# Kernel tuning notes

Hardware: AMD Instinct MI355X
Metric: run time of the kernel (lower is better)

The kernel has to match this reference:

```python
import jax, jax.numpy as jnp
import numpy as np

T, B, E, H = 2048, 2, 1024, 16
HD = E // H
NEG = -1e9  # large negative for causal additive mask


def setup_inputs() -> dict:
    key = jax.random.key(0)
    ks = jax.random.split(key, 6)
    s = 0.02
    query = jax.random.normal(ks[0], (T, B, E), jnp.float32)
    # causal additive mask, as commonly passed to this module's attn_mask arg
    attn_mask = jnp.triu(jnp.full((T, T), NEG, jnp.float32), k=1)
    key_padding_mask = jnp.zeros((B, T), jnp.bool_)
    Wq = jax.random.normal(ks[1], (E, E), jnp.float32) * s
    Wk = jax.random.normal(ks[2], (E, E), jnp.float32) * s
    Wv = jax.random.normal(ks[3], (E, E), jnp.float32) * s
    Wo = jax.random.normal(ks[4], (E, E), jnp.float32) * s
    bq = jnp.zeros((E,), jnp.float32)
    bk = jnp.zeros((E,), jnp.float32)
    bv = jnp.zeros((E,), jnp.float32)
    bo = jnp.zeros((E,), jnp.float32)
    return {"query": query, "attn_mask": attn_mask, "key_padding_mask": key_padding_mask,
            "Wq": Wq, "bq": bq, "Wk": Wk, "bk": bk, "Wv": Wv, "bv": bv, "Wo": Wo, "bo": bo}


def _shape(x):
    # [T, B, E] -> [B*H, T, HD]; E splits as (H, HD), flat index = b*H + h
    return x.reshape(T, B * H, HD).transpose(1, 0, 2)


def reference(query, attn_mask, key_padding_mask, Wq, bq, Wk, bk, Wv, bv, Wo, bo):
    scaling = HD ** -0.5
    q = (query @ Wq.T + bq) * scaling  # scale q as in torch code
    k = query @ Wk.T + bk              # self-attention path (static_kv=False)
    v = query @ Wv.T + bv
    q, k, v = _shape(q), _shape(k), _shape(v)            # [B*H, T, HD]
    w = jnp.einsum('bth,bsh->bts', q, k)                  # [B*H, T, S]
    w = w.reshape(B, H, T, T) + attn_mask                 # additive mask broadcast
    w = jnp.where(key_padding_mask[:, None, None, :], -jnp.inf, w)
    p = jax.nn.softmax(w, axis=-1).reshape(B * H, T, T)   # dropout p=0 (eval)
    o = jnp.einsum('bts,bsh->bth', p, v)                  # [B*H, T, HD]
    o = o.transpose(1, 0, 2).reshape(T, B, E)
    return o @ Wo.T + bo
```

## Files before the change

kernel.cpp:

```cpp
#include <hip/hip_runtime.h>

#define Tt 2048
#define Bb 2
#define Ee 1024
#define Hh 16
#define HD 64
#define BH 32

typedef __attribute__((ext_vector_type(8))) short short8;
typedef __attribute__((ext_vector_type(4))) short short4v;
typedef __attribute__((ext_vector_type(8))) __bf16 bf16x8;
typedef __attribute__((ext_vector_type(4))) float floatx4;

#define OFF_X  0
#define OFF_WQ 4194304
#define OFF_WK 5242880
#define OFF_WV 6291456
#define OFF_WO 7340032
#define OFF_Q  8388608
#define OFF_K  12582912
#define OFF_V  16777216
#define OFF_O  20971520

__device__ __forceinline__ short f2bf(float f) {
  union { float f; unsigned u; } a; a.f = f;
  unsigned r = a.u + 0x7fffu + ((a.u >> 16) & 1u);
  return (short)(r >> 16);
}

__device__ __forceinline__ floatx4 mfma16(short8 a, short8 b, floatx4 c) {
  return __builtin_amdgcn_mfma_f32_16x16x32_bf16(
      __builtin_bit_cast(bf16x8, a), __builtin_bit_cast(bf16x8, b), c, 0, 0, 0);
}

__device__ __forceinline__ void gl_lds16(const short* g, short* l) {
  __builtin_amdgcn_global_load_lds(
      (const __attribute__((address_space(1))) void*)g,
      (__attribute__((address_space(3))) void*)l, 16, 0, 0);
}

__device__ __forceinline__ uint2 exppack(floatx4 s, float& l) {
  float p0 = __builtin_amdgcn_exp2f(s[0]);
  float p1 = __builtin_amdgcn_exp2f(s[1]);
  float p2 = __builtin_amdgcn_exp2f(s[2]);
  float p3 = __builtin_amdgcn_exp2f(s[3]);
  l += (p0 + p1) + (p2 + p3);
  unsigned u0 = __builtin_bit_cast(unsigned, p0) + 0x8000u;
  unsigned u1 = __builtin_bit_cast(unsigned, p1) + 0x8000u;
  unsigned u2 = __builtin_bit_cast(unsigned, p2) + 0x8000u;
  unsigned u3 = __builtin_bit_cast(unsigned, p3) + 0x8000u;
  uint2 pk;
  pk.x = __builtin_amdgcn_perm(u1, u0, 0x07060302u);
  pk.y = __builtin_amdgcn_perm(u3, u2, 0x07060302u);
  return pk;
}

__global__ __launch_bounds__(256)
void convert_kernel(const float* __restrict__ x, const float* __restrict__ wq,
                    const float* __restrict__ wk, const float* __restrict__ wv,
                    const float* __restrict__ wo, short* __restrict__ dst)
{
  const int i4 = blockIdx.x * 256 + threadIdx.x;
  const int f = i4 * 4;
  const float* src;
  int local;
  if (f < 4194304) { src = x; local = f; }
  else {
    int gg = f - 4194304;
    int wsel = gg >> 20;
    local = gg & 1048575;
    src = (wsel == 0) ? wq : (wsel == 1) ? wk : (wsel == 2) ? wv : wo;
  }
  floatx4 v = *reinterpret_cast<const floatx4*>(src + local);
  short4 o;
  o.x = f2bf(v[0]); o.y = f2bf(v[1]); o.z = f2bf(v[2]); o.w = f2bf(v[3]);
  *reinterpret_cast<short4*>(dst + f) = o;
}

__global__ __launch_bounds__(256, 2)
void qkv_kernel(short* __restrict__ ws, const float* __restrict__ bq,
                const float* __restrict__ bk, const float* __restrict__ bv)
{
  __shared__ short smem[2][8192];
  const int t = threadIdx.x;
  const int lane = t & 63;
  const int w = t >> 6;
  const int g = lane >> 4, c = lane & 15;
  const int rb = blockIdx.x * 128;
  const int cb = blockIdx.y * 128;
  const int rw = (w >> 1) * 64, cw2 = (w & 1) * 64;

  const short* gA[2]; const short* gB[2]; int oC[2];
#pragma unroll
  for (int i = 0; i < 2; i++) {
    const int cid = t + 256 * i;
    const int row = cid >> 2;
    const int lch = (cid & 3) ^ ((row + (row >> 2)) & 3);
    gA[i] = ws + OFF_X + (rb + row) * 1024 + lch * 8;
    gB[i] = ws + OFF_WQ + (cb + row) * 1024 + lch * 8;
    oC[i] = cid * 8;
  }
  const int xr = (g ^ ((c + (c >> 2)) & 3)) * 8;

  floatx4 acc[4][4];
#pragma unroll
  for (int i = 0; i < 4; i++)
#pragma unroll
    for (int j = 0; j < 4; j++) acc[i][j] = (floatx4){0.f, 0.f, 0.f, 0.f};

#pragma unroll
  for (int i = 0; i < 2; i++) {
    gl_lds16(gA[i], &smem[0][oC[i]]);
    gl_lds16(gB[i], &smem[0][4096 + oC[i]]);
  }
  __syncthreads();

  for (int kt = 0; kt < 32; kt++) {
    const int cur = kt & 1;
    if (kt < 31) {
      const int kn = (kt + 1) * 32;
#pragma unroll
      for (int i = 0; i < 2; i++) {
        gl_lds16(gA[i] + kn, &smem[cur ^ 1][oC[i]]);
        gl_lds16(gB[i] + kn, &smem[cur ^ 1][4096 + oC[i]]);
      }
    }
    short8 af[4], bf[4];
#pragma unroll
    for (int mi = 0; mi < 4; mi++)
      af[mi] = *reinterpret_cast<const short8*>(&smem[cur][(rw + mi * 16 + c) * 32 + xr]);
#pragma unroll
    for (int ni = 0; ni < 4; ni++)
      bf[ni] = *reinterpret_cast<const short8*>(&smem[cur][4096 + (cw2 + ni * 16 + c) * 32 + xr]);
#pragma unroll
    for (int mi = 0; mi < 4; mi++)
#pragma unroll
      for (int ni = 0; ni < 4; ni++)
        acc[mi][ni] = mfma16(af[mi], bf[ni], acc[mi][ni]);
    __syncthreads();
  }

  const int m = cb >> 10;
  const int lcb = cb & 1023;
  if (m < 2) {
    short* vt = &smem[0][0];
    const float sc = (m == 0) ? 0.18033688f : 1.0f;
    const int baseo = (m == 0) ? OFF_Q : OFF_K;
    for (int hb = 0; hb < 2; hb++) {
      __syncthreads();
      if ((w >> 1) == hb) {
#pragma unroll
        for (int ni = 0; ni < 4; ni++) {
          const int lc = cw2 + ni * 16 + c;
          const float bcol = (m == 0 ? bq : bk)[lcb + lc];
#pragma unroll
          for (int mi = 0; mi < 4; mi++)
#pragma unroll
            for (int r = 0; r < 4; r++)
              vt[(mi * 16 + g * 4 + r) * 136 + lc] = f2bf((acc[mi][ni][r] + bcol) * sc);
        }
      }
      __syncthreads();
#pragma unroll
      for (int i = 0; i < 4; i++) {
        const int u = t + 256 * i;
        const int ttl = u & 31, bsel = (u >> 5) & 1, lc8 = u >> 6;
        const int rl = ttl * 2 + bsel;
        const int row = rb + hb * 64 + rl;
        const int tt = row >> 1, bb = row & 1;
        const int hh = (lcb + lc8 * 8) >> 6;
        short8 vv = *reinterpret_cast<const short8*>(vt + rl * 136 + lc8 * 8);
        *reinterpret_cast<short8*>(ws + baseo + (bb * Hh + hh) * 131072
            + (tt >> 4) * 1024 + (lc8 & 7) * 128 + (tt & 15) * 8) = vv;
      }
    }
  } else {
    short* vt = &smem[0][0];
    const int hb = lcb >> 6;
    for (int b = 0; b < 2; b++) {
      __syncthreads();
#pragma unroll
      for (int ni = 0; ni < 4; ni++) {
        const int lcol = cw2 + ni * 16 + c;
        const float bcol = bv[lcb + lcol];
#pragma unroll
        for (int mi = 0; mi < 4; mi++)
#pragma unroll
          for (int rr = 0; rr < 2; rr++) {
            const int r = rr * 2 + b;
            const int rloc = rw + mi * 16 + g * 4 + r;
            vt[lcol * 72 + (rloc >> 1)] = f2bf(acc[mi][ni][r] + bcol);
          }
      }
      __syncthreads();
#pragma unroll
      for (int i = 0; i < 4; i++) {
        const int u = t + 256 * i;
        const int lcol = u >> 3, seg = u & 7;
        short8 vv = *reinterpret_cast<const short8*>(vt + lcol * 72 + seg * 8);
        const int h = hb + (lcol >> 6), d = lcol & 63;
        *reinterpret_cast<short8*>(ws + OFF_V + ((b * Hh + h)) * 131072
                                   + ((rb >> 5) + (seg >> 1)) * 1024
                                   + d * 16 + (seg & 1) * 8) = vv;
      }
    }
  }
}

__global__ __launch_bounds__(256, 2)
void gemm_o(const short* __restrict__ ws, const float* __restrict__ bo,
            float* __restrict__ dout)
{
  __shared__ short smem[2][8192];
  const int t = threadIdx.x;
  const int lane = t & 63;
  const int w = t >> 6;
  const int g = lane >> 4, c = lane & 15;
  const int rb = blockIdx.x * 128;
  const int cb = blockIdx.y * 128;
  const int rw = (w >> 1) * 64, cw2 = (w & 1) * 64;

  const short* gA[2]; const short* gB[2]; int oC[2];
#pragma unroll
  for (int i = 0; i < 2; i++) {
    const int cid = t + 256 * i;
    const int row = cid >> 2;
    const int lch = (cid & 3) ^ ((row + (row >> 2)) & 3);
    gA[i] = ws + OFF_O + (rb + row) * 1024 + lch * 8;
    gB[i] = ws + OFF_WO + (cb + row) * 1024 + lch * 8;
    oC[i] = cid * 8;
  }
  const int xr = (g ^ ((c + (c >> 2)) & 3)) * 8;

  floatx4 acc[4][4];
#pragma unroll
  for (int i = 0; i < 4; i++)
#pragma unroll
    for (int j = 0; j < 4; j++) acc[i][j] = (floatx4){0.f, 0.f, 0.f, 0.f};

#pragma unroll
  for (int i = 0; i < 2; i++) {
    gl_lds16(gA[i], &smem[0][oC[i]]);
    gl_lds16(gB[i], &smem[0][4096 + oC[i]]);
  }
  __syncthreads();

  for (int kt = 0; kt < 32; kt++) {
    const int cur = kt & 1;
    if (kt < 31) {
      const int kn = (kt + 1) * 32;
#pragma unroll
      for (int i = 0; i < 2; i++) {
        gl_lds16(gA[i] + kn, &smem[cur ^ 1][oC[i]]);
        gl_lds16(gB[i] + kn, &smem[cur ^ 1][4096 + oC[i]]);
      }
    }
    short8 af[4], bf[4];
#pragma unroll
    for (int mi = 0; mi < 4; mi++)
      af[mi] = *reinterpret_cast<const short8*>(&smem[cur][(rw + mi * 16 + c) * 32 + xr]);
#pragma unroll
    for (int ni = 0; ni < 4; ni++)
      bf[ni] = *reinterpret_cast<const short8*>(&smem[cur][4096 + (cw2 + ni * 16 + c) * 32 + xr]);
#pragma unroll
    for (int mi = 0; mi < 4; mi++)
#pragma unroll
      for (int ni = 0; ni < 4; ni++)
        acc[mi][ni] = mfma16(af[mi], bf[ni], acc[mi][ni]);
    __syncthreads();
  }

#pragma unroll
  for (int ni = 0; ni < 4; ni++) {
    const int col = cb + cw2 + ni * 16 + c;
    const float bcol = bo[col];
#pragma unroll
    for (int mi = 0; mi < 4; mi++)
#pragma unroll
      for (int r = 0; r < 4; r++) {
        const int row = rb + rw + mi * 16 + g * 4 + r;
        dout[row * 1024 + col] = acc[mi][ni][r] + bcol;
      }
  }
}

__global__ __launch_bounds__(256, 3)
void attn_kernel(short* __restrict__ ws, const unsigned char* __restrict__ kpm)
{
  __shared__ __align__(16) short smem[24576];

  const int t = threadIdx.x;
  const int lane = t & 63;
  const int w = t >> 6;
  const int g = lane >> 4, c = lane & 15;
  const int bh = blockIdx.x;
  const int b = bh >> 4;
  const int h = bh & 15;
  const int qt = 31 - (int)blockIdx.y;
  const int qrow0 = qt * 64;

  const short* Qp = ws + OFF_Q + bh * 131072;
  const short* Kp = ws + OFF_K + bh * 131072;
  const short* Vp = ws + OFF_V + bh * 131072;

  short8 qf[4][2];
  const short* Qc = Qp + (qrow0 >> 4) * 1024 + lane * 8;
#pragma unroll
  for (int qs = 0; qs < 4; qs++) {
    qf[qs][0] = *reinterpret_cast<const short8*>(Qc + qs * 1024);
    qf[qs][1] = *reinterpret_cast<const short8*>(Qc + qs * 1024 + 512);
  }

  const uint4* kpv = reinterpret_cast<const uint4*>(kpm + b * Tt);
  uint4 k0v = kpv[lane * 2], k1v = kpv[lane * 2 + 1];
  const bool nz = (k0v.x | k0v.y | k0v.z | k0v.w | k1v.x | k1v.y | k1v.z | k1v.w) != 0;
  const unsigned long long kpany = __ballot(nz);

  float lt[4] = {0.f, 0.f, 0.f, 0.f};
  floatx4 acc[4][4];
#pragma unroll
  for (int i = 0; i < 4; i++)
#pragma unroll
    for (int j = 0; j < 4; j++) acc[i][j] = (floatx4){0.f, 0.f, 0.f, 0.f};

  const short* Ksrc = Kp + w * 1024 + lane * 8;
  const short* Vsrc = Vp + w * 1024 + lane * 8;
  const int woff = w * 1024;

  const int NT = qt + 1;
  const int NP = (NT + 1) >> 1;

  gl_lds16(Ksrc,       &smem[woff]);
  gl_lds16(Ksrc + 512, &smem[woff + 512]);
  gl_lds16(Vsrc,       &smem[4096 + woff]);
  gl_lds16(Vsrc + 512, &smem[4096 + woff + 512]);
  if (NT > 1) {
    gl_lds16(Ksrc + 4096,       &smem[8192 + woff]);
    gl_lds16(Ksrc + 4096 + 512, &smem[8192 + woff + 512]);
    gl_lds16(Vsrc + 4096,       &smem[8192 + 4096 + woff]);
    gl_lds16(Vsrc + 4096 + 512, &smem[8192 + 4096 + 512 + woff]);
  }

  int co = 0;
  for (int pp = 0; pp < NP; pp++) {
    const int ta = 2 * pp, tb = ta + 1;
    int cbuf = co + 8192;  if (cbuf >= 24576) cbuf -= 24576;
    int cn   = co + 16384; if (cn   >= 24576) cn   -= 24576;

    if (ta + 2 < NT) {
      const short* ks = Ksrc + (ta + 2) * 4096;
      const short* vs = Vsrc + (ta + 2) * 4096;
      gl_lds16(ks,       &smem[cn + woff]);
      gl_lds16(ks + 512, &smem[cn + woff + 512]);
      gl_lds16(vs,       &smem[cn + 4096 + woff]);
      gl_lds16(vs + 512, &smem[cn + 4096 + woff + 512]);
      asm volatile("s_waitcnt vmcnt(8)" ::: "memory");
    } else if (tb < NT) {
      asm volatile("s_waitcnt vmcnt(4)" ::: "memory");
    } else {
      asm volatile("s_waitcnt vmcnt(0)" ::: "memory");
    }
    __builtin_amdgcn_sched_barrier(0);

    const short* kfa = &smem[co + woff + g * 128 + c * 8];
    short8 ka0 = *reinterpret_cast<const short8*>(kfa);
    short8 ka1 = *reinterpret_cast<const short8*>(kfa + 512);
    __builtin_amdgcn_s_setprio(1);
    floatx4 sa[4];
#pragma unroll
    for (int qs = 0; qs < 4; qs++) {
      floatx4 z = (floatx4){0.f, 0.f, 0.f, 0.f};
      z = mfma16(ka0, qf[qs][0], z);
      z = mfma16(ka1, qf[qs][1], z);
      sa[qs] = z;
    }
    __builtin_amdgcn_s_setprio(0);
    if ((kpany >> (2 * ta)) & 3ULL) {
#pragma unroll
      for (int r = 0; r < 4; r++)
        if (kpm[b * Tt + ta * 64 + w * 16 + g * 4 + r] != 0) {
#pragma unroll
          for (int qs = 0; qs < 4; qs++) sa[qs][r] = -1e30f;
        }
    }
    if (ta == qt) {
      const int kl = w * 16 + g * 4;
#pragma unroll
      for (int qs = 0; qs < 4; qs++)
#pragma unroll
        for (int r = 0; r < 4; r++)
          if (kl + r > qs * 16 + c) sa[qs][r] = -1e30f;
    }
    uint2 ua[4];
#pragma unroll
    for (int qs = 0; qs < 4; qs++) ua[qs] = exppack(sa[qs], lt[qs]);
    const short* vfa = &smem[co + 4096 + woff + c * 16 + g * 4];
    short4v vA[4];
#pragma unroll
    for (int dt = 0; dt < 4; dt++)
      vA[dt] = *reinterpret_cast<const short4v*>(vfa + dt * 256);

    uint2 ub[4];
    ub[0] = ub[1] = ub[2] = ub[3] = (uint2){0u, 0u};
    short4v vB[4];
#pragma unroll
    for (int dt = 0; dt < 4; dt++) vB[dt] = vA[dt];
    if (tb < NT) {
      if (tb + 2 < NT) {
        const short* ks = Ksrc + (tb + 2) * 4096;
        const short* vs = Vsrc + (tb + 2) * 4096;
        gl_lds16(ks,       &smem[co + woff]);
        gl_lds16(ks + 512, &smem[co + woff + 512]);
        gl_lds16(vs,       &smem[co + 4096 + woff]);
        gl_lds16(vs + 512, &smem[co + 4096 + woff + 512]);
        asm volatile("s_waitcnt vmcnt(8)" ::: "memory");
      } else if (tb + 1 < NT) {
        asm volatile("s_waitcnt vmcnt(4)" ::: "memory");
      } else {
        asm volatile("s_waitcnt vmcnt(0)" ::: "memory");
      }
      __builtin_amdgcn_sched_barrier(0);

      const short* kfb = &smem[cbuf + woff + g * 128 + c * 8];
      short8 kb0 = *reinterpret_cast<const short8*>(kfb);
      short8 kb1 = *reinterpret_cast<const short8*>(kfb + 512);
      __builtin_amdgcn_s_setprio(1);
      floatx4 sb[4];
#pragma unroll
      for (int qs = 0; qs < 4; qs++) {
        floatx4 z = (floatx4){0.f, 0.f, 0.f, 0.f};
        z = mfma16(kb0, qf[qs][0], z);
        z = mfma16(kb1, qf[qs][1], z);
        sb[qs] = z;
      }
      __builtin_amdgcn_s_setprio(0);
      if ((kpany >> (2 * tb)) & 3ULL) {
#pragma unroll
        for (int r = 0; r < 4; r++)
          if (kpm[b * Tt + tb * 64 + w * 16 + g * 4 + r] != 0) {
#pragma unroll
            for (int qs = 0; qs < 4; qs++) sb[qs][r] = -1e30f;
          }
      }
      if (tb == qt) {
        const int kl = w * 16 + g * 4;
#pragma unroll
        for (int qs = 0; qs < 4; qs++)
#pragma unroll
          for (int r = 0; r < 4; r++)
            if (kl + r > qs * 16 + c) sb[qs][r] = -1e30f;
      }
#pragma unroll
      for (int qs = 0; qs < 4; qs++) ub[qs] = exppack(sb[qs], lt[qs]);
      const short* vfb = &smem[cbuf + 4096 + woff + c * 16 + g * 4];
#pragma unroll
      for (int dt = 0; dt < 4; dt++)
        vB[dt] = *reinterpret_cast<const short4v*>(vfb + dt * 256);
    }

    short8 pa8[4];
#pragma unroll
    for (int qs = 0; qs < 4; qs++) {
      uint4 uu; uu.x = ua[qs].x; uu.y = ua[qs].y; uu.z = ub[qs].x; uu.w = ub[qs].y;
      pa8[qs] = __builtin_bit_cast(short8, uu);
    }
    __builtin_amdgcn_s_setprio(1);
#pragma unroll
    for (int dt = 0; dt < 4; dt++) {
      short8 vv;
      vv[0] = vA[dt][0]; vv[1] = vA[dt][1]; vv[2] = vA[dt][2]; vv[3] = vA[dt][3];
      vv[4] = vB[dt][0]; vv[5] = vB[dt][1]; vv[6] = vB[dt][2]; vv[7] = vB[dt][3];
#pragma unroll
      for (int qs = 0; qs < 4; qs++)
        acc[qs][dt] = mfma16(pa8[qs], vv, acc[qs][dt]);
    }
    __builtin_amdgcn_s_setprio(0);

    co = cn;
  }

#pragma unroll
  for (int qs = 0; qs < 4; qs++) {
    lt[qs] += __shfl_xor(lt[qs], 16);
    lt[qs] += __shfl_xor(lt[qs], 32);
  }

  __syncthreads();
  float* bufA = reinterpret_cast<float*>(smem);
  float* bufB = bufA + 4352;
  float* Ls   = bufA + 8704;
  if (g == 0) {
#pragma unroll
    for (int qs = 0; qs < 4; qs++) Ls[w * 64 + qs * 16 + c] = lt[qs];
  }
  float* mybuf = (w < 2) ? bufA : bufB;
  if ((w & 1) == 0) {
#pragma unroll
    for (int qs = 0; qs < 4; qs++)
#pragma unroll
      for (int dt = 0; dt < 4; dt++)
#pragma unroll
        for (int r = 0; r < 4; r++)
          mybuf[(qs * 16 + g * 4 + r) * 68 + dt * 16 + c] = acc[qs][dt][r];
  }
  __syncthreads();
  if (w & 1) {
#pragma unroll
    for (int qs = 0; qs < 4; qs++)
#pragma unroll
      for (int dt = 0; dt < 4; dt++)
#pragma unroll
        for (int r = 0; r < 4; r++)
          mybuf[(qs * 16 + g * 4 + r) * 68 + dt * 16 + c] += acc[qs][dt][r];
  }
  __syncthreads();

  const int row = w * 16 + (lane >> 2);
  const int dseg = (lane & 3) * 16;
  const float inv = 1.f / (Ls[row] + Ls[64 + row] + Ls[128 + row] + Ls[192 + row]);
  short* op = ws + OFF_O + ((qrow0 + row) * Bb + b) * Ee + h * 64 + dseg;
#pragma unroll
  for (int i = 0; i < 2; i++) {
    floatx4 a0 = *reinterpret_cast<const floatx4*>(&bufA[row * 68 + dseg + i * 8]);
    floatx4 a1 = *reinterpret_cast<const floatx4*>(&bufA[row * 68 + dseg + i * 8 + 4]);
    floatx4 b0 = *reinterpret_cast<const floatx4*>(&bufB[row * 68 + dseg + i * 8]);
    floatx4 b1 = *reinterpret_cast<const floatx4*>(&bufB[row * 68 + dseg + i * 8 + 4]);
    short8 s;
#pragma unroll
    for (int j = 0; j < 4; j++) s[j] = f2bf((a0[j] + b0[j]) * inv);
#pragma unroll
    for (int j = 0; j < 4; j++) s[4 + j] = f2bf((a1[j] + b1[j]) * inv);
    *reinterpret_cast<short8*>(op + i * 8) = s;
  }
}

extern "C" void kernel_launch(void* const* d_in, const int* in_sizes, int n_in,
                              void* d_out, int out_size, void* d_ws, size_t ws_size,
                              hipStream_t stream)
{
  const float* query = (const float*)d_in[0];
  const unsigned char* kpm = (const unsigned char*)d_in[2];
  const float* Wq = (const float*)d_in[3];
  const float* bq = (const float*)d_in[4];
  const float* Wk = (const float*)d_in[5];
  const float* bk = (const float*)d_in[6];
  const float* Wv = (const float*)d_in[7];
  const float* bv = (const float*)d_in[8];
  const float* Wo = (const float*)d_in[9];
  const float* bo = (const float*)d_in[10];
  short* ws = (short*)d_ws;
  float* out = (float*)d_out;

  convert_kernel<<<dim3(8192), dim3(256), 0, stream>>>(query, Wq, Wk, Wv, Wo, ws);
  qkv_kernel<<<dim3(32, 24), dim3(256), 0, stream>>>(ws, bq, bk, bv);
  attn_kernel<<<dim3(32, 32), dim3(256), 0, stream>>>(ws, kpm);
  gemm_o<<<dim3(32, 8), dim3(256), 0, stream>>>(ws, bo, out);
}
```

Baseline: 181.8 us.

## Give each wave private LDS tiles in QKV GEMM to drop block barriers

The QKV projection GEMM now has each wave load its own 64-row A and B slices into a private LDS region, double-buffered, instead of the block sharing 128x32 tiles. This removes the per-iteration __syncthreads and replaces it with s_waitcnt vmcnt on the wave's own async loads. The cost is duplicated global loads (each A/B row is fetched by two waves), a 64KB LDS footprint that may reduce occupancy below the launch bound of 2 blocks, and the loss of the XOR swizzle, which may add LDS bank conflicts.

```diff
diff --git a/kernel.cpp b/kernel.cpp
--- a/kernel.cpp
+++ b/kernel.cpp
@@ -81,7 +81,7 @@
 void qkv_kernel(short* __restrict__ ws, const float* __restrict__ bq,
                 const float* __restrict__ bk, const float* __restrict__ bv)
 {
-  __shared__ short smem[2][8192];
+  __shared__ __align__(16) short smem[32768];
   const int t = threadIdx.x;
   const int lane = t & 63;
   const int w = t >> 6;
@@ -90,17 +90,9 @@
   const int cb = blockIdx.y * 128;
   const int rw = (w >> 1) * 64, cw2 = (w & 1) * 64;
 
-  const short* gA[2]; const short* gB[2]; int oC[2];
-#pragma unroll
-  for (int i = 0; i < 2; i++) {
-    const int cid = t + 256 * i;
-    const int row = cid >> 2;
-    const int lch = (cid & 3) ^ ((row + (row >> 2)) & 3);
-    gA[i] = ws + OFF_X + (rb + row) * 1024 + lch * 8;
-    gB[i] = ws + OFF_WQ + (cb + row) * 1024 + lch * 8;
-    oC[i] = cid * 8;
-  }
-  const int xr = (g ^ ((c + (c >> 2)) & 3)) * 8;
+  const short* srcA = ws + OFF_X  + (rb + rw  + (lane >> 2)) * 1024 + (lane & 3) * 8;
+  const short* srcB = ws + OFF_WQ + (cb + cw2 + (lane >> 2)) * 1024 + (lane & 3) * 8;
+  const int wbase = w * 4096;
 
   floatx4 acc[4][4];
 #pragma unroll
@@ -109,41 +101,47 @@
     for (int j = 0; j < 4; j++) acc[i][j] = (floatx4){0.f, 0.f, 0.f, 0.f};
 
 #pragma unroll
-  for (int i = 0; i < 2; i++) {
-    gl_lds16(gA[i], &smem[0][oC[i]]);
-    gl_lds16(gB[i], &smem[0][4096 + oC[i]]);
-  }
-  __syncthreads();
+  for (int j = 0; j < 4; j++) {
+    gl_lds16(srcA + j * 16384, &smem[wbase + j * 512]);
+    gl_lds16(srcB + j * 16384, &smem[wbase + 2048 + j * 512]);
+  }
 
   for (int kt = 0; kt < 32; kt++) {
-    const int cur = kt & 1;
+    const int co = (kt & 1) * 16384 + wbase;
     if (kt < 31) {
+      const int no = co ^ 16384;
       const int kn = (kt + 1) * 32;
 #pragma unroll
-      for (int i = 0; i < 2; i++) {
-        gl_lds16(gA[i] + kn, &smem[cur ^ 1][oC[i]]);
-        gl_lds16(gB[i] + kn, &smem[cur ^ 1][4096 + oC[i]]);
-      }
-    }
+      for (int j = 0; j < 4; j++) {
+        gl_lds16(srcA + j * 16384 + kn, &smem[no + j * 512]);
+        gl_lds16(srcB + j * 16384 + kn, &smem[no + 2048 + j * 512]);
+      }
+      asm volatile("s_waitcnt vmcnt(8)" ::: "memory");
+    } else {
+      asm volatile("s_waitcnt vmcnt(0)" ::: "memory");
+    }
+    __builtin_amdgcn_sched_barrier(0);
+
     short8 af[4], bf[4];
+    const short* pa = &smem[co + c * 32 + g * 8];
 #pragma unroll
     for (int mi = 0; mi < 4; mi++)
-      af[mi] = *reinterpret_cast<const short8*>(&smem[cur][(rw + mi * 16 + c) * 32 + xr]);
+      af[mi] = *reinterpret_cast<const short8*>(pa + mi * 512);
 #pragma unroll
     for (int ni = 0; ni < 4; ni++)
-      bf[ni] = *reinterpret_cast<const short8*>(&smem[cur][4096 + (cw2 + ni * 16 + c) * 32 + xr]);
+      bf[ni] = *reinterpret_cast<const short8*>(pa + 2048 + ni * 512);
 #pragma unroll
     for (int mi = 0; mi < 4; mi++)
 #pragma unroll
       for (int ni = 0; ni < 4; ni++)
         acc[mi][ni] = mfma16(af[mi], bf[ni], acc[mi][ni]);
-    __syncthreads();
+    __builtin_amdgcn_sched_barrier(0);
   }
 
   const int m = cb >> 10;
   const int lcb = cb & 1023;
   if (m < 2) {
-    short* vt = &smem[0][0];
+    short* vt = smem;
     const float sc = (m == 0) ? 0.18033688f : 1.0f;
     const int baseo = (m == 0) ? OFF_Q : OFF_K;
     for (int hb = 0; hb < 2; hb++) {
@@ -175,7 +173,7 @@
       }
     }
   } else {
-    short* vt = &smem[0][0];
+    short* vt = smem;
     const int hb = lcb >> 6;
     for (int b = 0; b < 2; b++) {
       __syncthreads();
```

Measured after the change: 195.0 us. 7.3% more time.
